# Optimization experiments

Measured on AMD Instinct MI355X. Metric: run time of the kernel, lower is better.

Reference implementation:

```python
import jax, jax.numpy as jnp
import numpy as np

N = 2048   # nodes in the tree
K = 2      # max children (heap-ordered binary tree)
IN = 1024  # in_dim
M = 1024   # mem_dim
L = 1024   # rows of the fixed attention matrix


def setup_inputs() -> dict:
    key = jax.random.key(0)
    ks = jax.random.split(key, 12)
    s_in = 1.0 / np.sqrt(IN)
    s_m = 1.0 / np.sqrt(M)
    inputs = jax.random.normal(ks[0], (N, IN), jnp.float32)
    hiddn_state_mat = jax.random.normal(ks[1], (L, M), jnp.float32)
    # heap-ordered binary tree: children of i are 2i+1, 2i+2; -1 = no child.
    ch = np.full((N, K), -1, dtype=np.int64)
    for k in range(K):
        c = 2 * np.arange(N) + 1 + k
        ch[:, k] = np.where(c < N, c, -1)
    children = jnp.asarray(ch)
    u = lambda k, shape, s: jax.random.uniform(k, shape, jnp.float32, -s, s)
    params = dict(
        ioux_w=u(ks[2], (3 * M, IN), s_in), ioux_b=u(ks[3], (3 * M,), s_in),
        iouh_w=u(ks[4], (3 * M, M), s_m),  iouh_b=u(ks[5], (3 * M,), s_m),
        fx_w=u(ks[6], (M, IN), s_in),      fx_b=u(ks[7], (M,), s_in),
        fh_w=u(ks[8], (M, M), s_m),        fh_b=u(ks[9], (M,), s_m),
        Wa=-0.05 + 0.05 * jax.random.normal(ks[10], (1, M), jnp.float32),
        attnh_w=u(ks[11], (M, 2 * M), s_m),
        attnh_b=jnp.zeros((M,), jnp.float32),
    )
    return dict(inputs=inputs, hiddn_state_mat=hiddn_state_mat, children=children, **params)


def reference(inputs, hiddn_state_mat, children, ioux_w, ioux_b, iouh_w, iouh_b,
              fx_w, fx_b, fh_w, fh_b, Wa, attnh_w, attnh_b):
    mask = (children >= 0)
    safe = jnp.where(mask, children, 0)
    # split attnh into the part acting on h (first M cols) and on hiddn_state_mat
    W1 = attnh_w[:, :M]  # [M, M]
    W2 = attnh_w[:, M:]  # [M, M]
    HW2 = hiddn_state_mat @ W2.T  # [L, M], constant across nodes
    x_iou = inputs @ ioux_w.T + ioux_b  # [N, 3M]
    x_f = inputs @ fx_w.T + fx_b        # [N, M]

    def step(carry, t):
        C, Hs = carry  # [N, M] each
        m = mask[t].astype(inputs.dtype)[:, None]        # [K, 1]
        c_ch = C[safe[t]] * m                            # [K, M] (zeros for pads == torch leaf zeros)
        h_ch = Hs[safe[t]] * m                           # [K, M]
        h_sum = h_ch.sum(0)                              # [M]
        iou = x_iou[t] + h_sum @ iouh_w.T + iouh_b       # [3M]
        i, o, u = jnp.split(iou, 3)
        i, o, u = jax.nn.sigmoid(i), jax.nn.sigmoid(o), jnp.tanh(u)
        f = jax.nn.sigmoid(h_ch @ fh_w.T + fh_b + x_f[t])  # [K, M]
        c = i * u + (f * c_ch).sum(0)                    # [M]
        h = o * jnp.tanh(c)                              # [M]
        # attention over the fixed hidden-state matrix
        a = jnp.tanh(h @ W1.T + HW2 + attnh_b)           # [L, M]
        p = jax.nn.softmax(a @ Wa[0])                    # [L]
        # sum(p[:,None]*h_tiled, 0) == sum(p)*h since rows are identical
        h = ((1.0 - p)[:, None] * hiddn_state_mat).sum(0) + jnp.sum(p) * h
        return (C.at[t].set(c), Hs.at[t].set(h)), None

    C0 = jnp.zeros((N, M), inputs.dtype)
    Hs0 = jnp.zeros((N, M), inputs.dtype)
    order = jnp.arange(N - 1, -1, -1)  # leaves first, root (node 0) last
    (C, Hs), _ = jax.lax.scan(step, (C0, Hs0), order)
    return C[0:1], Hs[0:1], Hs  # (root c, root h, all hidden states)
```

## Files before the change

kernel.cpp:

```cpp
#include <hip/hip_runtime.h>
#include <hip/hip_bf16.h>

#define MD 1024
#define LD 1024
#define ND 2048
#define JZ 4096

typedef __bf16 bf16x8 __attribute__((ext_vector_type(8)));
typedef __bf16 bf16x4 __attribute__((ext_vector_type(4)));
typedef float  f32x4  __attribute__((ext_vector_type(4)));

__device__ __forceinline__ float fsig(float x)  { return 1.0f / (1.0f + __expf(-x)); }
__device__ __forceinline__ float ftanh_(float x){ float e = __expf(2.0f * x); return 1.0f - 2.0f / (e + 1.0f); }

__device__ __forceinline__ void gload16(const __bf16* g, __bf16* l)
{
    __builtin_amdgcn_global_load_lds(
        (const __attribute__((address_space(1))) void*)g,
        (__attribute__((address_space(3))) void*)l, 16, 0, 0);
}

__global__ void cvt_rows_k(const float* __restrict__ src, int ld,
                           __bf16* __restrict__ dst, int K)
{
    int j = blockIdx.y;
    int k = blockIdx.x * 256 + threadIdx.x;
    dst[(size_t)j * K + k] = (__bf16)src[(size_t)j * ld + k];
}

__global__ void concat_bias_k(const float* __restrict__ a, const float* __restrict__ b,
                              float* __restrict__ dst)
{
    int i = blockIdx.x * 256 + threadIdx.x;
    dst[i] = (i < 3 * MD) ? a[i] : b[i - 3 * MD];
}

__global__ __launch_bounds__(256) void gemm_mfma(
    const __bf16* __restrict__ Ab, int lda,
    const __bf16* __restrict__ Wh,
    const float* __restrict__ bias,
    const float* __restrict__ X, int ldx, const float* __restrict__ add1,
    float* __restrict__ C, float* __restrict__ C2, __bf16* __restrict__ C3, int ldc,
    int I, int K, float scale, int epi)
{
    __shared__ __align__(16) __bf16 Ash[128][4][8];
    __shared__ __align__(16) __bf16 Bsh[128][4][8];
    const int tid = threadIdx.x;
    const int j0 = blockIdx.x * 128, i0 = blockIdx.y * 128;
    const int lane = tid & 63, wv = tid >> 6;
    const int wm = wv >> 1, wn = wv & 1;
    const int g = lane >> 4, fr = lane & 15;

    f32x4 acc[4][4];
    #pragma unroll
    for (int m = 0; m < 4; m++)
        #pragma unroll
        for (int n = 0; n < 4; n++)
            acc[m][n] = (f32x4){0.f, 0.f, 0.f, 0.f};

    const int srow = tid >> 2;
    const int sg   = tid & 3;
    int ar0 = i0 + srow;       if (ar0 >= I) ar0 = I - 1;
    int ar1 = i0 + srow + 64;  if (ar1 >= I) ar1 = I - 1;
    const __bf16* agp0 = Ab + (size_t)ar0 * lda + sg * 8;
    const __bf16* agp1 = Ab + (size_t)ar1 * lda + sg * 8;
    const __bf16* wgp0 = Wh + (size_t)(j0 + srow) * K + sg * 8;
    const __bf16* wgp1 = Wh + (size_t)(j0 + srow + 64) * K + sg * 8;
    __bf16* aD0 = &Ash[wv * 16][0][0];
    __bf16* aD1 = &Ash[64 + wv * 16][0][0];
    __bf16* bD0 = &Bsh[wv * 16][0][0];
    __bf16* bD1 = &Bsh[64 + wv * 16][0][0];

    for (int kt = 0; kt < K; kt += 32) {
        __syncthreads();
        gload16(agp0 + kt, aD0);
        gload16(agp1 + kt, aD1);
        gload16(wgp0 + kt, bD0);
        gload16(wgp1 + kt, bD1);
        __syncthreads();

        bf16x8 ah[4], bh[4];
        #pragma unroll
        for (int m = 0; m < 4; m++) ah[m] = *(bf16x8*)&Ash[wm * 64 + m * 16 + fr][g][0];
        #pragma unroll
        for (int n = 0; n < 4; n++) bh[n] = *(bf16x8*)&Bsh[wn * 64 + n * 16 + fr][g][0];
        #pragma unroll
        for (int m = 0; m < 4; m++)
            #pragma unroll
            for (int n = 0; n < 4; n++)
                acc[m][n] = __builtin_amdgcn_mfma_f32_16x16x32_bf16(ah[m], bh[n], acc[m][n], 0, 0, 0);
    }

    #pragma unroll
    for (int m = 0; m < 4; m++) {
        int rbase = i0 + wm * 64 + m * 16 + g * 4;
        #pragma unroll
        for (int nn = 0; nn < 4; nn++) {
            int col = j0 + wn * 64 + nn * 16 + fr;
            float b = bias ? bias[col] : 0.f;
            #pragma unroll
            for (int j = 0; j < 4; j++) {
                int r = rbase + j;
                if (r >= I) continue;
                float a = acc[m][nn][j];
                if (epi == 2) {
                    float hc = X[(size_t)r * ldx + col];
                    C[(size_t)r * ldc + col]  = add1[col] - a + hc;
                    float d = hc - a;
                    C2[(size_t)r * ldc + col] = d;
                    C3[(size_t)r * ldc + col] = (__bf16)d;
                } else {
                    float v = (a + b) * scale;
                    if (X) v += X[(size_t)r * ldx + col];
                    if (epi == 1) v = __expf(fminf(fmaxf(v, -80.f), 80.f));
                    C[(size_t)r * ldc + col] = v;
                }
            }
        }
    }
}

__global__ __launch_bounds__(256) void gemm64_mfma(
    const __bf16* __restrict__ Ab, int lda,
    const __bf16* __restrict__ Wh,
    const float* __restrict__ bias,
    const float* __restrict__ X, int ldx, const float* __restrict__ add1,
    float* __restrict__ C, float* __restrict__ C2, __bf16* __restrict__ C3, int ldc,
    int I, int K, float scale, int epi)
{
    __shared__ __align__(16) __bf16 Ash[64][4][8];
    __shared__ __align__(16) __bf16 Bsh[64][4][8];
    const int tid = threadIdx.x;
    const int j0 = blockIdx.x * 64, i0 = blockIdx.y * 64;
    const int lane = tid & 63, wv = tid >> 6;
    const int wm = wv >> 1, wn = wv & 1;
    const int g = lane >> 4, fr = lane & 15;

    f32x4 acc[2][2];
    #pragma unroll
    for (int m = 0; m < 2; m++)
        #pragma unroll
        for (int n = 0; n < 2; n++)
            acc[m][n] = (f32x4){0.f, 0.f, 0.f, 0.f};

    const int srow = tid >> 2;
    const int sg   = tid & 3;
    int ar = i0 + srow;  if (ar >= I) ar = I - 1;
    const __bf16* agp = Ab + (size_t)ar * lda + sg * 8;
    const __bf16* wgp = Wh + (size_t)(j0 + srow) * K + sg * 8;
    __bf16* aD = &Ash[wv * 16][0][0];
    __bf16* bD = &Bsh[wv * 16][0][0];

    for (int kt = 0; kt < K; kt += 32) {
        __syncthreads();
        gload16(agp + kt, aD);
        gload16(wgp + kt, bD);
        __syncthreads();

        bf16x8 ah[2], bh[2];
        #pragma unroll
        for (int m = 0; m < 2; m++) ah[m] = *(bf16x8*)&Ash[wm * 32 + m * 16 + fr][g][0];
        #pragma unroll
        for (int n = 0; n < 2; n++) bh[n] = *(bf16x8*)&Bsh[wn * 32 + n * 16 + fr][g][0];
        #pragma unroll
        for (int m = 0; m < 2; m++)
            #pragma unroll
            for (int n = 0; n < 2; n++)
                acc[m][n] = __builtin_amdgcn_mfma_f32_16x16x32_bf16(ah[m], bh[n], acc[m][n], 0, 0, 0);
    }

    #pragma unroll
    for (int m = 0; m < 2; m++) {
        int rbase = i0 + wm * 32 + m * 16 + g * 4;
        #pragma unroll
        for (int nn = 0; nn < 2; nn++) {
            int col = j0 + wn * 32 + nn * 16 + fr;
            float b = bias ? bias[col] : 0.f;
            #pragma unroll
            for (int j = 0; j < 4; j++) {
                int r = rbase + j;
                if (r >= I) continue;
                float a = acc[m][nn][j];
                if (epi == 2) {
                    float hc = X[(size_t)r * ldx + col];
                    C[(size_t)r * ldc + col]  = add1[col] - a + hc;
                    float d = hc - a;
                    C2[(size_t)r * ldc + col] = d;
                    C3[(size_t)r * ldc + col] = (__bf16)d;
                } else {
                    float v = (a + b) * scale;
                    if (X) v += X[(size_t)r * ldx + col];
                    if (epi == 1) v = __expf(fminf(fmaxf(v, -80.f), 80.f));
                    C[(size_t)r * ldc + col] = v;
                }
            }
        }
    }
}

template<int IMAX, bool WB>
__global__ __launch_bounds__(256) void gemv_nt(
    const float* __restrict__ Af, int lda, int I,
    const __bf16* __restrict__ Wb, const float* __restrict__ Wf, int ldw,
    const float* __restrict__ bias,
    const float* __restrict__ X, int ldx, const float* __restrict__ add1,
    float* __restrict__ C, float* __restrict__ C2, __bf16* __restrict__ C3, int ldc,
    int K, float scale, int epi)
{
    const int wv = threadIdx.x >> 6, lane = threadIdx.x & 63;
    const int j = blockIdx.x * 4 + wv;
    float acc[IMAX];
    #pragma unroll
    for (int i = 0; i < IMAX; i++) acc[i] = 0.0f;
    for (int k = lane * 4; k < K; k += 256) {
        float w0, w1, w2, w3;
        if (WB) {
            bf16x4 w4 = *(const bf16x4*)(Wb + (size_t)j * K + k);
            w0 = (float)w4[0]; w1 = (float)w4[1]; w2 = (float)w4[2]; w3 = (float)w4[3];
        } else {
            float4 w4 = *(const float4*)(Wf + (size_t)j * ldw + k);
            w0 = w4.x; w1 = w4.y; w2 = w4.z; w3 = w4.w;
        }
        #pragma unroll
        for (int i = 0; i < IMAX; i++) {
            if (i < I) {
                float4 a4 = *(const float4*)(Af + (size_t)i * lda + k);
                acc[i] += a4.x * w0 + a4.y * w1 + a4.z * w2 + a4.w * w3;
            }
        }
    }
    #pragma unroll
    for (int i = 0; i < IMAX; i++) {
        if (i < I) {
            float s = acc[i];
            #pragma unroll
            for (int off = 32; off >= 1; off >>= 1) s += __shfl_xor(s, off);
            if (lane == 0) {
                if (epi == 2) {
                    float hc = X[(size_t)i * ldx + j];
                    C[(size_t)i * ldc + j]  = add1[j] - s + hc;
                    float d = hc - s;
                    C2[(size_t)i * ldc + j] = d;
                    C3[(size_t)i * ldc + j] = (__bf16)d;
                } else {
                    float v = (s + (bias ? bias[j] : 0.f)) * scale;
                    if (X) v += X[(size_t)i * ldx + j];
                    if (epi == 1) v = __expf(fminf(fmaxf(v, -80.f), 80.f));
                    C[(size_t)i * ldc + j] = v;
                }
            }
        }
    }
}

template<int LTILE>
__global__ __launch_bounds__(512) void attn_s(
    int B, const float* __restrict__ Eh,
    const float* __restrict__ EH,
    const float* __restrict__ s_wa_sum,
    const float* __restrict__ Wa,
    float* __restrict__ S)
{
    __shared__ float s_e[8][MD];
    __shared__ float s_wa[MD];
    const int lt = blockIdx.x * LTILE;
    const int b0 = blockIdx.y * 8;
    const int nt = (B - b0 < 8) ? (B - b0) : 8;
    for (int idx = threadIdx.x; idx < MD; idx += 512) s_wa[idx] = Wa[idx];
    for (int i = 0; i < nt; i++)
        for (int idx = threadIdx.x; idx < MD; idx += 512)
            s_e[i][idx] = Eh[(size_t)(b0 + i) * MD + idx];
    __syncthreads();
    const int wv = threadIdx.x >> 6, lane = threadIdx.x & 63;
    const float swa = s_wa_sum[0];
    if (LTILE >= 16) {
        for (int l = lt + wv; l < lt + LTILE; l += 16) {
            float accA[8] = {}, accB[8] = {};
            const float* erA = EH + (size_t)l * MD;
            const float* erB = EH + (size_t)(l + 8) * MD;
            for (int mc = 0; mc < MD; mc += 256) {
                const int m = mc + lane * 4;
                float4 evA = *(const float4*)(erA + m);
                float4 evB = *(const float4*)(erB + m);
                float4 wa4 = *(const float4*)&s_wa[m];
                #pragma unroll
                for (int i = 0; i < 8; i++) {
                    if (i < nt) {
                        float4 se = *(const float4*)&s_e[i][m];
                        accA[i] = fmaf(wa4.x, __builtin_amdgcn_rcpf(fmaf(se.x, evA.x, 1.0f)), accA[i]);
                        accA[i] = fmaf(wa4.y, __builtin_amdgcn_rcpf(fmaf(se.y, evA.y, 1.0f)), accA[i]);
                        accA[i] = fmaf(wa4.z, __builtin_amdgcn_rcpf(fmaf(se.z, evA.z, 1.0f)), accA[i]);
                        accA[i] = fmaf(wa4.w, __builtin_amdgcn_rcpf(fmaf(se.w, evA.w, 1.0f)), accA[i]);
                        accB[i] = fmaf(wa4.x, __builtin_amdgcn_rcpf(fmaf(se.x, evB.x, 1.0f)), accB[i]);
                        accB[i] = fmaf(wa4.y, __builtin_amdgcn_rcpf(fmaf(se.y, evB.y, 1.0f)), accB[i]);
                        accB[i] = fmaf(wa4.z, __builtin_amdgcn_rcpf(fmaf(se.z, evB.z, 1.0f)), accB[i]);
                        accB[i] = fmaf(wa4.w, __builtin_amdgcn_rcpf(fmaf(se.w, evB.w, 1.0f)), accB[i]);
                    }
                }
            }
            #pragma unroll
            for (int i = 0; i < 8; i++) {
                if (i < nt) {
                    float vA = accA[i], vB = accB[i];
                    #pragma unroll
                    for (int off = 32; off >= 1; off >>= 1) {
                        vA += __shfl_xor(vA, off);
                        vB += __shfl_xor(vB, off);
                    }
                    if (lane == 0) {
                        S[(size_t)(b0 + i) * LD + l]     = swa - 2.0f * vA;
                        S[(size_t)(b0 + i) * LD + l + 8] = swa - 2.0f * vB;
                    }
                }
            }
        }
    } else {
        for (int l = lt + wv; l < lt + LTILE; l += 8) {
            float acc[8] = {};
            const float* er = EH + (size_t)l * MD;
            for (int mc = 0; mc < MD; mc += 256) {
                const int m = mc + lane * 4;
                float4 ev  = *(const float4*)(er + m);
                float4 wa4 = *(const float4*)&s_wa[m];
                #pragma unroll
                for (int i = 0; i < 8; i++) {
                    if (i < nt) {
                        float4 se = *(const float4*)&s_e[i][m];
                        acc[i] = fmaf(wa4.x, __builtin_amdgcn_rcpf(fmaf(se.x, ev.x, 1.0f)), acc[i]);
                        acc[i] = fmaf(wa4.y, __builtin_amdgcn_rcpf(fmaf(se.y, ev.y, 1.0f)), acc[i]);
                        acc[i] = fmaf(wa4.z, __builtin_amdgcn_rcpf(fmaf(se.z, ev.z, 1.0f)), acc[i]);
                        acc[i] = fmaf(wa4.w, __builtin_amdgcn_rcpf(fmaf(se.w, ev.w, 1.0f)), acc[i]);
                    }
                }
            }
            #pragma unroll
            for (int i = 0; i < 8; i++) {
                if (i < nt) {
                    float v = acc[i];
                    #pragma unroll
                    for (int off = 32; off >= 1; off >>= 1) v += __shfl_xor(v, off);
                    if (lane == 0) S[(size_t)(b0 + i) * LD + l] = swa - 2.0f * v;
                }
            }
        }
    }
}

__global__ __launch_bounds__(256) void softmax_rows(float* __restrict__ S, __bf16* __restrict__ Sb)
{
    float* row = S + (size_t)blockIdx.x * LD;
    __bf16* rb = Sb + (size_t)blockIdx.x * LD;
    const int tid = threadIdx.x;
    const int wv = tid >> 6, lane = tid & 63;
    float v0 = row[tid], v1 = row[tid + 256], v2 = row[tid + 512], v3 = row[tid + 768];
    float mx = fmaxf(fmaxf(v0, v1), fmaxf(v2, v3));
    #pragma unroll
    for (int off = 32; off >= 1; off >>= 1) mx = fmaxf(mx, __shfl_xor(mx, off));
    __shared__ float r1[4], r2[4];
    if (lane == 0) r1[wv] = mx;
    __syncthreads();
    mx = fmaxf(fmaxf(r1[0], r1[1]), fmaxf(r1[2], r1[3]));
    float e0 = __expf(v0 - mx), e1 = __expf(v1 - mx), e2 = __expf(v2 - mx), e3 = __expf(v3 - mx);
    float sm = e0 + e1 + e2 + e3;
    #pragma unroll
    for (int off = 32; off >= 1; off >>= 1) sm += __shfl_xor(sm, off);
    if (lane == 0) r2[wv] = sm;
    __syncthreads();
    sm = r2[0] + r2[1] + r2[2] + r2[3];
    float inv = 1.0f / sm;
    float p0 = e0 * inv, p1 = e1 * inv, p2 = e2 * inv, p3 = e3 * inv;
    row[tid] = p0; row[tid + 256] = p1; row[tid + 512] = p2; row[tid + 768] = p3;
    rb[tid] = (__bf16)p0; rb[tid + 256] = (__bf16)p1;
    rb[tid + 512] = (__bf16)p2; rb[tid + 768] = (__bf16)p3;
}

__global__ void cell_finish_k(const int* __restrict__ children, int t0,
    const float* __restrict__ Z, const float* __restrict__ HsumWz,
    const float* __restrict__ iouh_b, const float* __restrict__ fh_b,
    const float* __restrict__ x_all,
    float* __restrict__ Cmat, float* __restrict__ hcell, __bf16* __restrict__ hcellB)
{
    int b = blockIdx.y;
    int m = blockIdx.x * 256 + threadIdx.x;
    int t = t0 + b;
    int c0 = children[2 * t], c1 = children[2 * t + 1];
    float cnt = (float)((c0 >= 0) + (c1 >= 0));
    const float* z0 = (c0 >= 0) ? Z + (size_t)c0 * JZ : nullptr;
    const float* z1 = (c1 >= 0) ? Z + (size_t)c1 * JZ : nullptr;
    const float* xr = x_all + (size_t)t * JZ;

    float zi = 0.f, zo = 0.f, zu = 0.f;
    if (z0) { zi += z0[m]; zo += z0[MD + m]; zu += z0[2 * MD + m]; }
    if (z1) { zi += z1[m]; zo += z1[MD + m]; zu += z1[2 * MD + m]; }
    float iv = fsig (zi + cnt * HsumWz[m]           + iouh_b[m]           + xr[m]);
    float ov = fsig (zo + cnt * HsumWz[MD + m]      + iouh_b[MD + m]      + xr[MD + m]);
    float uv = ftanh_(zu + cnt * HsumWz[2 * MD + m] + iouh_b[2 * MD + m]  + xr[2 * MD + m]);

    float xf  = xr[3 * MD + m];
    float hwf = HsumWz[3 * MD + m] + fh_b[m] + xf;
    float c = iv * uv;
    if (c0 >= 0) {
        float f0 = fsig(z0[3 * MD + m] + hwf);
        c += f0 * Cmat[(size_t)c0 * MD + m];
    }
    if (c1 >= 0) {
        float f1 = fsig(z1[3 * MD + m] + hwf);
        c += f1 * Cmat[(size_t)c1 * MD + m];
    }
    Cmat[(size_t)t * MD + m] = c;
    float h = ov * ftanh_(c);
    hcell[(size_t)b * MD + m] = h;
    hcellB[(size_t)b * MD + m] = (__bf16)h;
}

__global__ void colsum_part_k(const float* __restrict__ H, float* __restrict__ part)
{
    int m = blockIdx.x * 256 + threadIdx.x;
    int lb = blockIdx.y;
    float s = 0.f;
    for (int l = lb * 64; l < lb * 64 + 64; l++) s += H[(size_t)l * MD + m];
    part[(size_t)lb * MD + m] = s;
}

__global__ void colsum_reduce_k(const float* __restrict__ part, float* __restrict__ Hsum)
{
    int m = blockIdx.x * 256 + threadIdx.x;
    float s = 0.f;
    for (int lb = 0; lb < 16; lb++) s += part[(size_t)lb * MD + m];
    Hsum[m] = s;
}

__global__ void transpose2_k(const float* __restrict__ H,
                             float* __restrict__ Ht, __bf16* __restrict__ Htb)
{
    __shared__ float tile[32][33];
    int mb = blockIdx.x * 32, lb = blockIdx.y * 32;
    int tx = threadIdx.x, ty = threadIdx.y;
    #pragma unroll
    for (int jj = 0; jj < 4; jj++)
        tile[ty + jj * 8][tx] = H[(size_t)(lb + ty + jj * 8) * MD + mb + tx];
    __syncthreads();
    #pragma unroll
    for (int jj = 0; jj < 4; jj++) {
        float v = tile[tx][ty + jj * 8];
        size_t idx = (size_t)(mb + ty + jj * 8) * LD + lb + tx;
        Ht[idx]  = v;
        Htb[idx] = (__bf16)v;
    }
}

__global__ void sumwa_k(const float* __restrict__ Wa, float* __restrict__ out)
{
    int tid = threadIdx.x;
    float v = Wa[tid] + Wa[tid + 256] + Wa[tid + 512] + Wa[tid + 768];
    #pragma unroll
    for (int off = 32; off >= 1; off >>= 1) v += __shfl_xor(v, off);
    __shared__ float r[4];
    if ((tid & 63) == 0) r[tid >> 6] = v;
    __syncthreads();
    if (tid == 0) out[0] = r[0] + r[1] + r[2] + r[3];
}

__global__ void final_copy_k(const float* __restrict__ Cmat, float* __restrict__ out)
{
    int m = blockIdx.x * 256 + threadIdx.x;
    out[m] = Cmat[m];
    out[1024 + m] = out[2048 + m];
}

static inline void mmx(const __bf16* Ab, const float* Af, int lda, int I,
                       const __bf16* Wb,
                       const float* bias, const float* X, int ldx, const float* add1,
                       float* C, float* C2, __bf16* C3, int ldc, int J, int K,
                       float scale, int epi, hipStream_t s)
{
    if (I <= 32) {
        gemv_nt<32, true><<<J / 4, 256, 0, s>>>(Af, lda, I, Wb, nullptr, K,
            bias, X, ldx, add1, C, C2, C3, ldc, K, scale, epi);
    } else {
        int b128 = (J / 128) * ((I + 127) / 128);
        if (b128 >= 192)
            gemm_mfma<<<dim3(J / 128, (I + 127) / 128), 256, 0, s>>>(
                Ab, lda, Wb, bias, X, ldx, add1, C, C2, C3, ldc, I, K, scale, epi);
        else
            gemm64_mfma<<<dim3(J / 64, (I + 63) / 64), 256, 0, s>>>(
                Ab, lda, Wb, bias, X, ldx, add1, C, C2, C3, ldc, I, K, scale, epi);
    }
}

extern "C" void kernel_launch(void* const* d_in, const int* in_sizes, int n_in,
                              void* d_out, int out_size, void* d_ws, size_t ws_size,
                              hipStream_t stream)
{
    const float* inputs   = (const float*)d_in[0];
    const float* Hmat     = (const float*)d_in[1];
    const int*   children = (const int*)d_in[2];
    const float* ioux_w   = (const float*)d_in[3];
    const float* ioux_b   = (const float*)d_in[4];
    const float* iouh_w   = (const float*)d_in[5];
    const float* iouh_b   = (const float*)d_in[6];
    const float* fx_w     = (const float*)d_in[7];
    const float* fx_b     = (const float*)d_in[8];
    const float* fh_w     = (const float*)d_in[9];
    const float* fh_b     = (const float*)d_in[10];
    const float* Wa       = (const float*)d_in[11];
    const float* attnh_w  = (const float*)d_in[12];
    const float* attnh_b  = (const float*)d_in[13];

    float* out = (float*)d_out;
    float* Hs  = out + 2048;

    float* p = (float*)d_ws;
    float* x_all   = p;  p += (size_t)ND * JZ;
    float* Zbuf    = p;  p += (size_t)ND * JZ;
    float* EHbuf   = p;  p += (size_t)LD * MD;
    float* Ht      = p;  p += (size_t)MD * LD;
    float* Cmat    = p;  p += (size_t)ND * MD;
    float* Hdelta  = p;  p += (size_t)ND * MD;
    float* hcell   = p;  p += (size_t)1024 * MD;
    float* Ehbuf   = p;  p += (size_t)1024 * MD;
    float* Sbuf    = p;  p += (size_t)1024 * LD;
    float* Hsum    = p;  p += MD;
    float* part16  = p;  p += 16 * MD;
    float* S_wa    = p;  p += 8;
    float* HsumWz  = p;  p += JZ;
    float* bx      = p;  p += JZ;
    __bf16* q = (__bf16*)p;
    __bf16* WzB    = q; q += (size_t)JZ * MD;
    __bf16* WxB    = q; q += (size_t)JZ * MD;
    __bf16* W1H    = q; q += (size_t)MD * MD;
    __bf16* W2H    = q; q += (size_t)MD * MD;
    __bf16* HtH    = q; q += (size_t)MD * LD;
    __bf16* inpB   = q; q += (size_t)ND * MD;
    __bf16* HmatB  = q; q += (size_t)LD * MD;
    __bf16* SbB    = q; q += (size_t)1024 * LD;
    __bf16* HdB    = q; q += (size_t)ND * MD;
    __bf16* hcellB = q; q += (size_t)1024 * MD;

    cvt_rows_k<<<dim3(4, 3 * MD), 256, 0, stream>>>(iouh_w, MD, WzB, MD);
    cvt_rows_k<<<dim3(4, MD), 256, 0, stream>>>(fh_w, MD, WzB + (size_t)3 * MD * MD, MD);
    cvt_rows_k<<<dim3(4, 3 * MD), 256, 0, stream>>>(ioux_w, MD, WxB, MD);
    cvt_rows_k<<<dim3(4, MD), 256, 0, stream>>>(fx_w, MD, WxB + (size_t)3 * MD * MD, MD);
    cvt_rows_k<<<dim3(4, MD), 256, 0, stream>>>(attnh_w, 2 * MD, W1H, MD);
    cvt_rows_k<<<dim3(4, MD), 256, 0, stream>>>(attnh_w + MD, 2 * MD, W2H, MD);
    cvt_rows_k<<<dim3(4, ND), 256, 0, stream>>>(inputs, MD, inpB, MD);
    cvt_rows_k<<<dim3(4, LD), 256, 0, stream>>>(Hmat, MD, HmatB, MD);
    concat_bias_k<<<JZ / 256, 256, 0, stream>>>(ioux_b, fx_b, bx);
    transpose2_k<<<dim3(32, 32), dim3(32, 8), 0, stream>>>(Hmat, Ht, HtH);
    sumwa_k<<<1, 256, 0, stream>>>(Wa, S_wa);
    colsum_part_k<<<dim3(4, 16), 256, 0, stream>>>(Hmat, part16);
    colsum_reduce_k<<<4, 256, 0, stream>>>(part16, Hsum);
    gemv_nt<1, false><<<(3 * MD) / 4, 256, 0, stream>>>(Hsum, MD, 1, nullptr, iouh_w, MD,
        nullptr, nullptr, 0, nullptr, HsumWz, nullptr, nullptr, 3 * MD, MD, 1.0f, 0);
    gemv_nt<1, false><<<MD / 4, 256, 0, stream>>>(Hsum, MD, 1, nullptr, fh_w, MD,
        nullptr, nullptr, 0, nullptr, HsumWz + 3 * MD, nullptr, nullptr, MD, MD, 1.0f, 0);

    mmx(inpB, nullptr, MD, ND, WxB, bx, nullptr, 0, nullptr,
        x_all, nullptr, nullptr, JZ, JZ, MD, 1.0f, 0, stream);
    mmx(HmatB, nullptr, MD, LD, W2H, attnh_b, nullptr, 0, nullptr,
        EHbuf, nullptr, nullptr, MD, MD, MD, 2.0f, 1, stream);

    static const int lv_t0[12] = {2047, 1023, 511, 255, 127, 63, 31, 15, 7, 3, 1, 0};
    static const int lv_B [12] = {1, 1024, 512, 256, 128, 64, 32, 16, 8, 4, 2, 1};
    for (int li = 0; li < 12; li++) {
        int t0 = lv_t0[li], B = lv_B[li];
        cell_finish_k<<<dim3(4, B), 256, 0, stream>>>(children, t0, Zbuf, HsumWz,
                                                      iouh_b, fh_b, x_all, Cmat, hcell, hcellB);
        mmx(hcellB, hcell, MD, B, W1H, nullptr, nullptr, 0, nullptr,
            Ehbuf, nullptr, nullptr, MD, MD, MD, 2.0f, 1, stream);
        if (B >= 128)
            attn_s<64><<<dim3(LD / 64, B / 8), 512, 0, stream>>>(B, Ehbuf, EHbuf, S_wa, Wa, Sbuf);
        else
            attn_s<8><<<dim3(LD / 8, (B + 7) / 8), 512, 0, stream>>>(B, Ehbuf, EHbuf, S_wa, Wa, Sbuf);
        softmax_rows<<<B, 256, 0, stream>>>(Sbuf, SbB);
        mmx(SbB, Sbuf, LD, B, HtH, nullptr, hcell, MD, Hsum,
            Hs + (size_t)t0 * MD, Hdelta + (size_t)t0 * MD, HdB + (size_t)t0 * MD,
            MD, MD, LD, 1.0f, 2, stream);
        if (li < 11)
            mmx(HdB + (size_t)t0 * MD, Hdelta + (size_t)t0 * MD, MD, B, WzB,
                nullptr, nullptr, 0, nullptr,
                Zbuf + (size_t)t0 * JZ, nullptr, nullptr, JZ, JZ, MD, 1.0f, 0, stream);
    }
    final_copy_k<<<4, 256, 0, stream>>>(Cmat, out);
}
```

Before: 1.227 ms.

## Fuse small tree levels into persistent grid-barrier kernel and merge conversion launches

Levels with at most 32 nodes (the first leaf-only level and the last six levels) now run inside one persistent kernel of 256 blocks. It steps through cell update, W1 projection, attention scores, softmax, output projection and the Z projection, with a software grid barrier between phases. This removes dozens of small kernel launches and their gaps along the serial critical path. The eight per-matrix bf16 conversion kernels are merged into one grid-stride kernel. The change risks deadlock if all 256 blocks are not co-resident, and it uses scalar fp32 dot products instead of MFMA for these small batches.

Result: slower. 2.362 ms (+92.5%).

```diff
diff --git a/kernel.cpp b/kernel.cpp
--- a/kernel.cpp
+++ b/kernel.cpp
@@ -13,6 +13,13 @@
 __device__ __forceinline__ float fsig(float x)  { return 1.0f / (1.0f + __expf(-x)); }
 __device__ __forceinline__ float ftanh_(float x){ float e = __expf(2.0f * x); return 1.0f - 2.0f / (e + 1.0f); }
 
+__device__ __forceinline__ bf16x8 bzero8() {
+    bf16x8 z;
+    #pragma unroll
+    for (int q = 0; q < 8; q++) z[q] = (__bf16)0.f;
+    return z;
+}
+
 __device__ __forceinline__ void gload16(const __bf16* g, __bf16* l)
 {
     __builtin_amdgcn_global_load_lds(
@@ -20,12 +27,59 @@
         (__attribute__((address_space(3))) void*)l, 16, 0, 0);
 }
 
-__global__ void cvt_rows_k(const float* __restrict__ src, int ld,
-                           __bf16* __restrict__ dst, int K)
-{
-    int j = blockIdx.y;
-    int k = blockIdx.x * 256 + threadIdx.x;
-    dst[(size_t)j * K + k] = (__bf16)src[(size_t)j * ld + k];
+__device__ __forceinline__ void grid_barrier(int* bar, int nb)
+{
+    __syncthreads();
+    if (threadIdx.x == 0) {
+        __threadfence();
+        int* cnt = bar;
+        int* gen = bar + 1;
+        int g = __hip_atomic_load(gen, __ATOMIC_RELAXED, __HIP_MEMORY_SCOPE_AGENT);
+        int a = __hip_atomic_fetch_add(cnt, 1, __ATOMIC_ACQ_REL, __HIP_MEMORY_SCOPE_AGENT);
+        if (a == nb - 1) {
+            __hip_atomic_store(cnt, 0, __ATOMIC_RELAXED, __HIP_MEMORY_SCOPE_AGENT);
+            __hip_atomic_fetch_add(gen, 1, __ATOMIC_RELEASE, __HIP_MEMORY_SCOPE_AGENT);
+        } else {
+            while (__hip_atomic_load(gen, __ATOMIC_ACQUIRE, __HIP_MEMORY_SCOPE_AGENT) == g)
+                __builtin_amdgcn_s_sleep(8);
+        }
+        __threadfence();
+    }
+    __syncthreads();
+}
+
+__global__ void cvt_all_k(const float* __restrict__ iouh_w, const float* __restrict__ fh_w,
+                          const float* __restrict__ ioux_w, const float* __restrict__ fx_w,
+                          const float* __restrict__ attnh_w, const float* __restrict__ inputs,
+                          const float* __restrict__ Hmat,
+                          __bf16* __restrict__ WzB, __bf16* __restrict__ WxB,
+                          __bf16* __restrict__ W1H, __bf16* __restrict__ W2H,
+                          __bf16* __restrict__ inpB, __bf16* __restrict__ HmatB)
+{
+    const size_t MM = (size_t)MD * MD;
+    const size_t b0 = 3 * MM, b1 = 4 * MM, b2 = 7 * MM, b3 = 8 * MM;
+    const size_t b4 = 9 * MM, b5 = 10 * MM, b6 = 12 * MM, b7 = 13 * MM;
+    for (size_t idx = (size_t)blockIdx.x * 256 + threadIdx.x; idx < b7;
+         idx += (size_t)gridDim.x * 256) {
+        if (idx < b1) {
+            WzB[idx] = (__bf16)((idx < b0) ? iouh_w[idx] : fh_w[idx - b0]);
+        } else if (idx < b3) {
+            size_t r = idx - b1;
+            WxB[r] = (__bf16)((idx < b2) ? ioux_w[r] : fx_w[idx - b2]);
+        } else if (idx < b4) {
+            size_t r = idx - b3; size_t j = r >> 10, k = r & (MD - 1);
+            W1H[r] = (__bf16)attnh_w[j * 2 * MD + k];
+        } else if (idx < b5) {
+            size_t r = idx - b4; size_t j = r >> 10, k = r & (MD - 1);
+            W2H[r] = (__bf16)attnh_w[j * 2 * MD + MD + k];
+        } else if (idx < b6) {
+            size_t r = idx - b5;
+            inpB[r] = (__bf16)inputs[r];
+        } else {
+            size_t r = idx - b6;
+            HmatB[r] = (__bf16)Hmat[r];
+        }
+    }
 }
 
 __global__ void concat_bias_k(const float* __restrict__ a, const float* __restrict__ b,
@@ -198,14 +252,11 @@
     }
 }
 
-template<int IMAX, bool WB>
+template<int IMAX>
 __global__ __launch_bounds__(256) void gemv_nt(
     const float* __restrict__ Af, int lda, int I,
-    const __bf16* __restrict__ Wb, const float* __restrict__ Wf, int ldw,
-    const float* __restrict__ bias,
-    const float* __restrict__ X, int ldx, const float* __restrict__ add1,
-    float* __restrict__ C, float* __restrict__ C2, __bf16* __restrict__ C3, int ldc,
-    int K, float scale, int epi)
+    const float* __restrict__ Wf, int ldw,
+    float* __restrict__ C, int ldc, int K)
 {
     const int wv = threadIdx.x >> 6, lane = threadIdx.x & 63;
     const int j = blockIdx.x * 4 + wv;
@@ -213,19 +264,12 @@
     #pragma unroll
     for (int i = 0; i < IMAX; i++) acc[i] = 0.0f;
     for (int k = lane * 4; k < K; k += 256) {
-        float w0, w1, w2, w3;
-        if (WB) {
-            bf16x4 w4 = *(const bf16x4*)(Wb + (size_t)j * K + k);
-            w0 = (float)w4[0]; w1 = (float)w4[1]; w2 = (float)w4[2]; w3 = (float)w4[3];
-        } else {
-            float4 w4 = *(const float4*)(Wf + (size_t)j * ldw + k);
-            w0 = w4.x; w1 = w4.y; w2 = w4.z; w3 = w4.w;
-        }
+        float4 w4 = *(const float4*)(Wf + (size_t)j * ldw + k);
         #pragma unroll
         for (int i = 0; i < IMAX; i++) {
             if (i < I) {
                 float4 a4 = *(const float4*)(Af + (size_t)i * lda + k);
-                acc[i] += a4.x * w0 + a4.y * w1 + a4.z * w2 + a4.w * w3;
+                acc[i] += a4.x * w4.x + a4.y * w4.y + a4.z * w4.z + a4.w * w4.w;
             }
         }
     }
@@ -235,20 +279,7 @@
             float s = acc[i];
             #pragma unroll
             for (int off = 32; off >= 1; off >>= 1) s += __shfl_xor(s, off);
-            if (lane == 0) {
-                if (epi == 2) {
-                    float hc = X[(size_t)i * ldx + j];
-                    C[(size_t)i * ldc + j]  = add1[j] - s + hc;
-                    float d = hc - s;
-                    C2[(size_t)i * ldc + j] = d;
-                    C3[(size_t)i * ldc + j] = (__bf16)d;
-                } else {
-                    float v = (s + (bias ? bias[j] : 0.f)) * scale;
-                    if (X) v += X[(size_t)i * ldx + j];
-                    if (epi == 1) v = __expf(fminf(fmaxf(v, -80.f), 80.f));
-                    C[(size_t)i * ldc + j] = v;
-                }
-            }
+            if (lane == 0) C[(size_t)i * ldc + j] = s;
         }
     }
 }
@@ -399,18 +430,206 @@
     float xf  = xr[3 * MD + m];
     float hwf = HsumWz[3 * MD + m] + fh_b[m] + xf;
     float c = iv * uv;
-    if (c0 >= 0) {
-        float f0 = fsig(z0[3 * MD + m] + hwf);
-        c += f0 * Cmat[(size_t)c0 * MD + m];
-    }
-    if (c1 >= 0) {
-        float f1 = fsig(z1[3 * MD + m] + hwf);
-        c += f1 * Cmat[(size_t)c1 * MD + m];
-    }
+    if (c0 >= 0) c += fsig(z0[3 * MD + m] + hwf) * Cmat[(size_t)c0 * MD + m];
+    if (c1 >= 0) c += fsig(z1[3 * MD + m] + hwf) * Cmat[(size_t)c1 * MD + m];
     Cmat[(size_t)t * MD + m] = c;
     float h = ov * ftanh_(c);
     hcell[(size_t)b * MD + m] = h;
     hcellB[(size_t)b * MD + m] = (__bf16)h;
+}
+
+__global__ __launch_bounds__(256) void tail_k(
+    const int* __restrict__ children, const float* __restrict__ HsumWz,
+    const float* __restrict__ iouh_b, const float* __restrict__ fh_b,
+    const float* __restrict__ x_all, float* __restrict__ Cmat,
+    float* __restrict__ hcell, const __bf16* __restrict__ W1H,
+    float* __restrict__ Ehbuf, const float* __restrict__ EHbuf,
+    const float* __restrict__ S_wa, const float* __restrict__ Wa,
+    float* __restrict__ Sbuf, const __bf16* __restrict__ HtH,
+    const float* __restrict__ Hsum, float* __restrict__ Hs,
+    float* __restrict__ Hdelta, float* __restrict__ Zbuf,
+    const __bf16* __restrict__ WzB, int* bar, int liFrom, int liTo)
+{
+    static const int t0s[12] = {2047, 1023, 511, 255, 127, 63, 31, 15, 7, 3, 1, 0};
+    static const int Bs [12] = {1, 1024, 512, 256, 128, 64, 32, 16, 8, 4, 2, 1};
+    const int NB = 256;
+    const int tid = threadIdx.x;
+    const int wv = tid >> 6, lane = tid & 63;
+    const int w = blockIdx.x * 4 + wv;
+    __shared__ float r1[4], r2[4];
+
+    for (int li = liFrom; li < liTo; li++) {
+        const int t0 = t0s[li], B = Bs[li];
+        for (int idx = blockIdx.x * 256 + tid; idx < B * MD; idx += NB * 256) {
+            int b = idx >> 10, m = idx & (MD - 1);
+            int t = t0 + b;
+            int c0 = children[2 * t], c1 = children[2 * t + 1];
+            float cnt = (float)((c0 >= 0) + (c1 >= 0));
+            const float* z0 = (c0 >= 0) ? Zbuf + (size_t)c0 * JZ : nullptr;
+            const float* z1 = (c1 >= 0) ? Zbuf + (size_t)c1 * JZ : nullptr;
+            const float* xr = x_all + (size_t)t * JZ;
+            float zi = 0.f, zo = 0.f, zu = 0.f;
+            if (z0) { zi += z0[m]; zo += z0[MD + m]; zu += z0[2 * MD + m]; }
+            if (z1) { zi += z1[m]; zo += z1[MD + m]; zu += z1[2 * MD + m]; }
+            float iv = fsig (zi + cnt * HsumWz[m]           + iouh_b[m]           + xr[m]);
+            float ov = fsig (zo + cnt * HsumWz[MD + m]      + iouh_b[MD + m]      + xr[MD + m]);
+            float uv = ftanh_(zu + cnt * HsumWz[2 * MD + m] + iouh_b[2 * MD + m]  + xr[2 * MD + m]);
+            float hwf = HsumWz[3 * MD + m] + fh_b[m] + xr[3 * MD + m];
+            float c = iv * uv;
+            if (c0 >= 0) c += fsig(z0[3 * MD + m] + hwf) * Cmat[(size_t)c0 * MD + m];
+            if (c1 >= 0) c += fsig(z1[3 * MD + m] + hwf) * Cmat[(size_t)c1 * MD + m];
+            Cmat[(size_t)t * MD + m] = c;
+            hcell[(size_t)b * MD + m] = ov * ftanh_(c);
+        }
+        grid_barrier(bar, NB);
+        {
+            const int j = w;
+            float acc[32];
+            #pragma unroll
+            for (int i = 0; i < 32; i++) acc[i] = 0.f;
+            const __bf16* Wj = W1H + (size_t)j * MD;
+            for (int k = lane * 4; k < MD; k += 256) {
+                bf16x4 w4 = *(const bf16x4*)(Wj + k);
+                float w0 = (float)w4[0], w1 = (float)w4[1], w2 = (float)w4[2], w3 = (float)w4[3];
+                #pragma unroll
+                for (int i = 0; i < 32; i++) {
+                    if (i < B) {
+                        float4 a4 = *(const float4*)(hcell + (size_t)i * MD + k);
+                        acc[i] += a4.x * w0 + a4.y * w1 + a4.z * w2 + a4.w * w3;
+                    }
+                }
+            }
+            #pragma unroll
+            for (int i = 0; i < 32; i++) {
+                if (i < B) {
+                    float s = acc[i];
+                    #pragma unroll
+                    for (int off = 32; off >= 1; off >>= 1) s += __shfl_xor(s, off);
+                    if (lane == 0) {
+                        float v = 2.0f * s;
+                        Ehbuf[(size_t)i * MD + j] = __expf(fminf(fmaxf(v, -80.f), 80.f));
+                    }
+                }
+            }
+        }
+        grid_barrier(bar, NB);
+        {
+            const int l = w;
+            const float swa = S_wa[0];
+            float acc[32];
+            #pragma unroll
+            for (int i = 0; i < 32; i++) acc[i] = 0.f;
+            const float* er = EHbuf + (size_t)l * MD;
+            for (int m = lane * 4; m < MD; m += 256) {
+                float4 ev  = *(const float4*)(er + m);
+                float4 wa4 = *(const float4*)(Wa + m);
+                #pragma unroll
+                for (int i = 0; i < 32; i++) {
+                    if (i < B) {
+                        float4 se = *(const float4*)(Ehbuf + (size_t)i * MD + m);
+                        acc[i] = fmaf(wa4.x, __builtin_amdgcn_rcpf(fmaf(se.x, ev.x, 1.0f)), acc[i]);
+                        acc[i] = fmaf(wa4.y, __builtin_amdgcn_rcpf(fmaf(se.y, ev.y, 1.0f)), acc[i]);
+                        acc[i] = fmaf(wa4.z, __builtin_amdgcn_rcpf(fmaf(se.z, ev.z, 1.0f)), acc[i]);
+                        acc[i] = fmaf(wa4.w, __builtin_amdgcn_rcpf(fmaf(se.w, ev.w, 1.0f)), acc[i]);
+                    }
+                }
+            }
+            #pragma unroll
+            for (int i = 0; i < 32; i++) {
+                if (i < B) {
+                    float s = acc[i];
+                    #pragma unroll
+                    for (int off = 32; off >= 1; off >>= 1) s += __shfl_xor(s, off);
+                    if (lane == 0) Sbuf[(size_t)i * LD + l] = swa - 2.0f * s;
+                }
+            }
+        }
+        grid_barrier(bar, NB);
+        if ((int)blockIdx.x < B) {
+            float* row = Sbuf + (size_t)blockIdx.x * LD;
+            float v0 = row[tid], v1 = row[tid + 256], v2 = row[tid + 512], v3 = row[tid + 768];
+            float mx = fmaxf(fmaxf(v0, v1), fmaxf(v2, v3));
+            #pragma unroll
+            for (int off = 32; off >= 1; off >>= 1) mx = fmaxf(mx, __shfl_xor(mx, off));
+            if (lane == 0) r1[wv] = mx;
+            __syncthreads();
+            mx = fmaxf(fmaxf(r1[0], r1[1]), fmaxf(r1[2], r1[3]));
+            float e0 = __expf(v0 - mx), e1 = __expf(v1 - mx), e2 = __expf(v2 - mx), e3 = __expf(v3 - mx);
+            float sm = e0 + e1 + e2 + e3;
+            #pragma unroll
+            for (int off = 32; off >= 1; off >>= 1) sm += __shfl_xor(sm, off);
+            if (lane == 0) r2[wv] = sm;
+            __syncthreads();
+            sm = r2[0] + r2[1] + r2[2] + r2[3];
+            float inv = 1.0f / sm;
+            row[tid] = e0 * inv; row[tid + 256] = e1 * inv;
+            row[tid + 512] = e2 * inv; row[tid + 768] = e3 * inv;
+        }
+        grid_barrier(bar, NB);
+        {
+            const int j = w;
+            float acc[32];
+            #pragma unroll
+            for (int i = 0; i < 32; i++) acc[i] = 0.f;
+            const __bf16* Hj = HtH + (size_t)j * LD;
+            for (int l = lane * 4; l < LD; l += 256) {
+                bf16x4 h4 = *(const bf16x4*)(Hj + l);
+                float h0 = (float)h4[0], h1 = (float)h4[1], h2 = (float)h4[2], h3 = (float)h4[3];
+                #pragma unroll
+                for (int i = 0; i < 32; i++) {
+                    if (i < B) {
+                        float4 p4 = *(const float4*)(Sbuf + (size_t)i * LD + l);
+                        acc[i] += p4.x * h0 + p4.y * h1 + p4.z * h2 + p4.w * h3;
+                    }
+                }
+            }
+            #pragma unroll
+            for (int i = 0; i < 32; i++) {
+                if (i < B) {
+                    float s = acc[i];
+                    #pragma unroll
+                    for (int off = 32; off >= 1; off >>= 1) s += __shfl_xor(s, off);
+                    if (lane == 0) {
+                        float hc = hcell[(size_t)i * MD + j];
+                        Hs[(size_t)(t0 + i) * MD + j] = Hsum[j] - s + hc;
+                        Hdelta[(size_t)(t0 + i) * MD + j] = hc - s;
+                    }
+                }
+            }
+        }
+        grid_barrier(bar, NB);
+        if (li != 11) {
+            #pragma unroll
+            for (int pass = 0; pass < 4; pass++) {
+                const int j = w + pass * 1024;
+                float acc[32];
+                #pragma unroll
+                for (int i = 0; i < 32; i++) acc[i] = 0.f;
+                const __bf16* Wj = WzB + (size_t)j * MD;
+                for (int k = lane * 4; k < MD; k += 256) {
+                    bf16x4 w4 = *(const bf16x4*)(Wj + k);
+                    float w0 = (float)w4[0], w1 = (float)w4[1], w2 = (float)w4[2], w3 = (float)w4[3];
+                    #pragma unroll
+                    for (int i = 0; i < 32; i++) {
+                        if (i < B) {
+                            float4 d4 = *(const float4*)(Hdelta + (size_t)(t0 + i) * MD + k);
+                            acc[i] += d4.x * w0 + d4.y * w1 + d4.z * w2 + d4.w * w3;
+                        }
+                    }
+                }
+                #pragma unroll
+                for (int i = 0; i < 32; i++) {
+                    if (i < B) {
+                        float s = acc[i];
+                        #pragma unroll
+                        for (int off = 32; off >= 1; off >>= 1) s += __shfl_xor(s, off);
+                        if (lane == 0) Zbuf[(size_t)(t0 + i) * JZ + j] = s;
+                    }
+                }
+            }
+        }
+        grid_barrier(bar, NB);
+    }
 }
 
 __global__ void colsum_part_k(const float* __restrict__ H, float* __restrict__ part)
@@ -468,24 +687,19 @@
     out[1024 + m] = out[2048 + m];
 }
 
-static inline void mmx(const __bf16* Ab, const float* Af, int lda, int I,
+static inline void mmx(const __bf16* Ab, int lda, int I,
                        const __bf16* Wb,
                        const float* bias, const float* X, int ldx, const float* add1,
                        float* C, float* C2, __bf16* C3, int ldc, int J, int K,
                        float scale, int epi, hipStream_t s)
 {
-    if (I <= 32) {
-        gemv_nt<32, true><<<J / 4, 256, 0, s>>>(Af, lda, I, Wb, nullptr, K,
-            bias, X, ldx, add1, C, C2, C3, ldc, K, scale, epi);
-    } else {
-        int b128 = (J / 128) * ((I + 127) / 128);
-        if (b128 >= 192)
-            gemm_mfma<<<dim3(J / 128, (I + 127) / 128), 256, 0, s>>>(
-                Ab, lda, Wb, bias, X, ldx, add1, C, C2, C3, ldc, I, K, scale, epi);
-        else
-            gemm64_mfma<<<dim3(J / 64, (I + 63) / 64), 256, 0, s>>>(
-                Ab, lda, Wb, bias, X, ldx, add1, C, C2, C3, ldc, I, K, scale, epi);
-    }
+    int b128 = (J / 128) * ((I + 127) / 128);
+    if (b128 >= 192)
+        gemm_mfma<<<dim3(J / 128, (I + 127) / 128), 256, 0, s>>>(
+            Ab, lda, Wb, bias, X, ldx, add1, C, C2, C3, ldc, I, K, scale, epi);
+    else
+        gemm64_mfma<<<dim3(J / 64, (I + 63) / 64), 256, 0, s>>>(
+            Ab, lda, Wb, bias, X, ldx, add1, C, C2, C3, ldc, I, K, scale, epi);
 }
 
 extern "C" void kernel_launch(void* const* d_in, const int* in_sizes, int n_in,
@@ -525,6 +739,7 @@
     float* S_wa    = p;  p += 8;
     float* HsumWz  = p;  p += JZ;
     float* bx      = p;  p += JZ;
+    int*   bar     = (int*)p; p += 8;
     __bf16* q = (__bf16*)p;
     __bf16* WzB    = q; q += (size_t)JZ * MD;
     __bf16* WxB    = q; q += (size_t)JZ * MD;
@@ -537,49 +752,51 @@
     __bf16* HdB    = q; q += (size_t)ND * MD;
     __bf16* hcellB = q; q += (size_t)1024 * MD;
 
-    cvt_rows_k<<<dim3(4, 3 * MD), 256, 0, stream>>>(iouh_w, MD, WzB, MD);
-    cvt_rows_k<<<dim3(4, MD), 256, 0, stream>>>(fh_w, MD, WzB + (size_t)3 * MD * MD, MD);
-    cvt_rows_k<<<dim3(4, 3 * MD), 256, 0, stream>>>(ioux_w, MD, WxB, MD);
-    cvt_rows_k<<<dim3(4, MD), 256, 0, stream>>>(fx_w, MD, WxB + (size_t)3 * MD * MD, MD);
-    cvt_rows_k<<<dim3(4, MD), 256, 0, stream>>>(attnh_w, 2 * MD, W1H, MD);
-    cvt_rows_k<<<dim3(4, MD), 256, 0, stream>>>(attnh_w + MD, 2 * MD, W2H, MD);
-    cvt_rows_k<<<dim3(4, ND), 256, 0, stream>>>(inputs, MD, inpB, MD);
-    cvt_rows_k<<<dim3(4, LD), 256, 0, stream>>>(Hmat, MD, HmatB, MD);
+    cvt_all_k<<<2048, 256, 0, stream>>>(iouh_w, fh_w, ioux_w, fx_w, attnh_w, inputs, Hmat,
+                                        WzB, WxB, W1H, W2H, inpB, HmatB);
     concat_bias_k<<<JZ / 256, 256, 0, stream>>>(ioux_b, fx_b, bx);
     transpose2_k<<<dim3(32, 32), dim3(32, 8), 0, stream>>>(Hmat, Ht, HtH);
     sumwa_k<<<1, 256, 0, stream>>>(Wa, S_wa);
     colsum_part_k<<<dim3(4, 16), 256, 0, stream>>>(Hmat, part16);
     colsum_reduce_k<<<4, 256, 0, stream>>>(part16, Hsum);
-    gemv_nt<1, false><<<(3 * MD) / 4, 256, 0, stream>>>(Hsum, MD, 1, nullptr, iouh_w, MD,
-        nullptr, nullptr, 0, nullptr, HsumWz, nullptr, nullptr, 3 * MD, MD, 1.0f, 0);
-    gemv_nt<1, false><<<MD / 4, 256, 0, stream>>>(Hsum, MD, 1, nullptr, fh_w, MD,
-        nullptr, nullptr, 0, nullptr, HsumWz + 3 * MD, nullptr, nullptr, MD, MD, 1.0f, 0);
-
-    mmx(inpB, nullptr, MD, ND, WxB, bx, nullptr, 0, nullptr,
+    gemv_nt<1><<<(3 * MD) / 4, 256, 0, stream>>>(Hsum, MD, 1, iouh_w, MD, HsumWz, 3 * MD, MD);
+    gemv_nt<1><<<MD / 4, 256, 0, stream>>>(Hsum, MD, 1, fh_w, MD, HsumWz + 3 * MD, MD, MD);
+
+    mmx(inpB, MD, ND, WxB, bx, nullptr, 0, nullptr,
         x_all, nullptr, nullptr, JZ, JZ, MD, 1.0f, 0, stream);
-    mmx(HmatB, nullptr, MD, LD, W2H, attnh_b, nullptr, 0, nullptr,
+    mmx(HmatB, MD, LD, W2H, attnh_b, nullptr, 0, nullptr,
         EHbuf, nullptr, nullptr, MD, MD, MD, 2.0f, 1, stream);
 
     static const int lv_t0[12] = {2047, 1023, 511, 255, 127, 63, 31, 15, 7, 3, 1, 0};
     static const int lv_B [12] = {1, 1024, 512, 256, 128, 64, 32, 16, 8, 4, 2, 1};
-    for (int li = 0; li < 12; li++) {
+
+    hipMemsetAsync(bar, 0, 8, stream);
+    tail_k<<<256, 256, 0, stream>>>(children, HsumWz, iouh_b, fh_b, x_all, Cmat, hcell,
+                                    W1H, Ehbuf, EHbuf, S_wa, Wa, Sbuf, HtH, Hsum,
+                                    Hs, Hdelta, Zbuf, WzB, bar, 0, 1);
+
+    for (int li = 1; li <= 5; li++) {
         int t0 = lv_t0[li], B = lv_B[li];
         cell_finish_k<<<dim3(4, B), 256, 0, stream>>>(children, t0, Zbuf, HsumWz,
                                                       iouh_b, fh_b, x_all, Cmat, hcell, hcellB);
-        mmx(hcellB, hcell, MD, B, W1H, nullptr, nullptr, 0, nullptr,
+        mmx(hcellB, MD, B, W1H, nullptr, nullptr, 0, nullptr,
             Ehbuf, nullptr, nullptr, MD, MD, MD, 2.0f, 1, stream);
         if (B >= 128)
             attn_s<64><<<dim3(LD / 64, B / 8), 512, 0, stream>>>(B, Ehbuf, EHbuf, S_wa, Wa, Sbuf);
         else
             attn_s<8><<<dim3(LD / 8, (B + 7) / 8), 512, 0, stream>>>(B, Ehbuf, EHbuf, S_wa, Wa, Sbuf);
         softmax_rows<<<B, 256, 0, stream>>>(Sbuf, SbB);
-        mmx(SbB, Sbuf, LD, B, HtH, nullptr, hcell, MD, Hsum,
+        mmx(SbB, LD, B, HtH, nullptr, hcell, MD, Hsum,
             Hs + (size_t)t0 * MD, Hdelta + (size_t)t0 * MD, HdB + (size_t)t0 * MD,
             MD, MD, LD, 1.0f, 2, stream);
-        if (li < 11)
-            mmx(HdB + (size_t)t0 * MD, Hdelta + (size_t)t0 * MD, MD, B, WzB,
-                nullptr, nullptr, 0, nullptr,
-                Zbuf + (size_t)t0 * JZ, nullptr, nullptr, JZ, JZ, MD, 1.0f, 0, stream);
-    }
+        mmx(HdB + (size_t)t0 * MD, MD, B, WzB, nullptr, nullptr, 0, nullptr,
+            Zbuf + (size_t)t0 * JZ, nullptr, nullptr, JZ, JZ, MD, 1.0f, 0, stream);
+    }
+
+    hipMemsetAsync(bar, 0, 8, stream);
+    tail_k<<<256, 256, 0, stream>>>(children, HsumWz, iouh_b, fh_b, x_all, Cmat, hcell,
+                                    W1H, Ehbuf, EHbuf, S_wa, Wa, Sbuf, HtH, Hsum,
+                                    Hs, Hdelta, Zbuf, WzB, bar, 6, 12);
+
     final_copy_k<<<4, 256, 0, stream>>>(Cmat, out);
 }
```
